# Kernel tuning notes

Hardware: AMD Instinct MI355X
Metric: run time of the kernel (lower is better)

## Reference

```python
import jax, jax.numpy as jnp
import numpy as np

N_USERS = 100000
N_ITEMS = 100000
D_FEAT = 256
BATCH = 8192
CLASSES = 5
E = 500000
D_CONV = 128
D_RAW = 256
D_EMB = 256
NUM_BASIS = 2
BN_EPS = 1e-3  # tf.contrib.layers.batch_norm default epsilon


def _bn_params(key, dim):
    # packed [gamma, beta, moving_mean, moving_var]
    return jnp.stack([jnp.ones(dim), jnp.zeros(dim), jnp.zeros(dim), jnp.ones(dim)]).astype(jnp.float32)


def setup_inputs() -> dict:
    key = jax.random.key(0)
    ks = jax.random.split(key, 24)
    s = lambda fan_in, fan_out: np.sqrt(2.0 / (fan_in + fan_out)).astype(np.float32)
    inp = {
        'user_feat': jax.random.normal(ks[0], (N_USERS, D_FEAT), jnp.float32),
        'item_feat': jax.random.normal(ks[1], (N_ITEMS, D_FEAT), jnp.float32),
        'user_idx': jax.random.randint(ks[2], (BATCH,), 0, N_USERS, jnp.int32),
        'item_idx': jax.random.randint(ks[3], (BATCH,), 0, N_ITEMS, jnp.int32),
        'user_edge_src': jax.random.randint(ks[4], (CLASSES, E), 0, N_ITEMS, jnp.int32),
        'user_edge_dst': jax.random.randint(ks[5], (CLASSES, E), 0, BATCH, jnp.int32),
        'user_edge_w': jax.random.uniform(ks[6], (CLASSES, E), jnp.float32),
        'item_edge_src': jax.random.randint(ks[7], (CLASSES, E), 0, N_USERS, jnp.int32),
        'item_edge_dst': jax.random.randint(ks[8], (CLASSES, E), 0, BATCH, jnp.int32),
        'item_edge_w': jax.random.uniform(ks[9], (CLASSES, E), jnp.float32),
        'W_fu': jax.random.normal(ks[10], (D_FEAT, D_RAW), jnp.float32) * s(D_FEAT, D_RAW),
        'b_fu': jnp.zeros((D_RAW,), jnp.float32),
        'W_fi': jax.random.normal(ks[11], (D_FEAT, D_RAW), jnp.float32) * s(D_FEAT, D_RAW),
        'b_fi': jnp.zeros((D_RAW,), jnp.float32),
        'W_uc': jax.random.normal(ks[12], (CLASSES, D_FEAT, D_CONV), jnp.float32) * s(D_FEAT, D_CONV),
        'W_ic': jax.random.normal(ks[13], (CLASSES, D_FEAT, D_CONV), jnp.float32) * s(D_FEAT, D_CONV),
        'bn_fu': _bn_params(ks[14], D_RAW),
        'bn_hu': _bn_params(ks[15], CLASSES * D_CONV),
        'bn_fi': _bn_params(ks[16], D_RAW),
        'bn_hi': _bn_params(ks[17], CLASSES * D_CONV),
        'W2_fu': jax.random.normal(ks[18], (D_RAW, D_EMB), jnp.float32) * s(D_RAW, D_EMB),
        'W2_hu': jax.random.normal(ks[19], (CLASSES * D_CONV, D_EMB), jnp.float32) * s(CLASSES * D_CONV, D_EMB),
        'W2_fi': jax.random.normal(ks[20], (D_RAW, D_EMB), jnp.float32) * s(D_RAW, D_EMB),
        'W2_hi': jax.random.normal(ks[21], (CLASSES * D_CONV, D_EMB), jnp.float32) * s(CLASSES * D_CONV, D_EMB),
        'Wdec': jax.random.normal(ks[22], (NUM_BASIS, D_EMB, D_EMB), jnp.float32) * s(D_EMB, D_EMB),
        'Wcomb': jax.random.normal(ks[23], (CLASSES, NUM_BASIS), jnp.float32) * s(CLASSES, NUM_BASIS),
    }
    return inp


def _bn(x, p):
    gamma, beta, mean, var = p[0], p[1], p[2], p[3]
    return gamma * (x - mean) * jax.lax.rsqrt(var + BN_EPS) + beta


def _agg(feat, src, dst, w, n_rows):
    # weighted sparse [B, N] x dense [N, D] aggregation via gather + segment_sum
    msgs = feat[src] * w[:, None]  # [E, D]
    return jax.ops.segment_sum(msgs, dst, num_segments=n_rows)


def reference(user_feat, item_feat, user_idx, item_idx,
              user_edge_src, user_edge_dst, user_edge_w,
              item_edge_src, item_edge_dst, item_edge_w,
              W_fu, b_fu, W_fi, b_fi, W_uc, W_ic,
              bn_fu, bn_hu, bn_fi, bn_hi,
              W2_fu, W2_hu, W2_fi, W2_hi, Wdec, Wcomb):
    B = user_idx.shape[0]
    classes = W_uc.shape[0]

    # batch row selection (sparse.matmul with one-hot selector == gather)
    f_user = user_feat[user_idx] @ W_fu + b_fu  # [B, D_RAW]
    f_item = item_feat[item_idx] @ W_fi + b_fi

    # per-class graph convolution: aggregate opposite-side features, project, stack
    h_user = jnp.concatenate(
        [_agg(item_feat, user_edge_src[c], user_edge_dst[c], user_edge_w[c], B) @ W_uc[c]
         for c in range(classes)], axis=1)  # [B, classes*D_CONV]
    h_item = jnp.concatenate(
        [_agg(user_feat, item_edge_src[c], item_edge_dst[c], item_edge_w[c], B) @ W_ic[c]
         for c in range(classes)], axis=1)

    # batchnorm (inference stats) + relu  (dropout rate 0 -> identity)
    f_user = jax.nn.relu(_bn(f_user, bn_fu))
    f_item = jax.nn.relu(_bn(f_item, bn_fi))
    h_user = jax.nn.relu(_bn(h_user, bn_hu))
    h_item = jax.nn.relu(_bn(h_item, bn_hi))

    user_emb = jax.nn.relu(f_user @ W2_fu + h_user @ W2_hu)  # [B, D_EMB]
    item_emb = jax.nn.relu(f_item @ W2_fi + h_item @ W2_hi)

    # bilinear decoder: per-class kernel = sum_k Wcomb[r,k] * Wdec[k]
    kernels = jnp.einsum('rk,kij->rij', Wcomb, Wdec)  # [classes, D_EMB, D_EMB]
    logits = jnp.einsum('bi,rij,bj->br', user_emb, kernels, item_emb)  # [B, classes]
    return logits


if __name__ == '__main__':
    out = reference(**setup_inputs())
    print(out.shape, out.dtype)
```

## Files before the change

### kernel.cpp

```cpp
#include <hip/hip_runtime.h>
#include <cstdint>
#include <cstddef>

#define NBATCH   8192
#define DFEAT    256
#define DCONV    128
#define NCLASS   5
#define NEDGE    500000
#define NUSERS   100000
#define BN_EPS   1e-3f
#define NBUCKET  128
#define BROWS    64
#define CAP      4608
#define NPHB     16
#define NPHU     13

typedef unsigned short u16;
typedef short bf16x8_t __attribute__((ext_vector_type(8)));
typedef float f32x4_t  __attribute__((ext_vector_type(4)));

__device__ __forceinline__ u16 f2bf(float x) {
    unsigned u = __float_as_uint(x);
    u += 0x7FFF + ((u >> 16) & 1);
    return (u16)(u >> 16);
}
__device__ __forceinline__ float bf2f(u16 h) {
    return __uint_as_float(((unsigned)h) << 16);
}

template<int AF32>
__device__ __forceinline__ void mfma_tiles_t(
    const void* __restrict__ Av, int lda, const int* __restrict__ gather,
    const u16* __restrict__ BT, int K,
    int tileM, int tileN, u16* As, u16* Bs, f32x4_t acc[4])
{
    const int t    = threadIdx.x;
    const int rowi = t >> 2;
    const int kc   = t & 3;
    const int w    = t >> 6;
    const int lane = t & 63;

    int ar = gather ? gather[tileM + rowi] : (tileM + rowi);
    const u16*   Ap16 = (const u16*)Av   + (size_t)ar * lda + kc * 8;
    const float* Apf  = (const float*)Av + (size_t)ar * lda + kc * 8;
    const u16* Bp = BT + (size_t)(tileN + rowi) * K + kc * 8;
    u16* Aw = As + (size_t)(((rowi >> 4) * 64) + (rowi & 15) + 16 * kc) * 8;
    u16* Bw = Bs + (size_t)(((rowi >> 4) * 64) + (rowi & 15) + 16 * kc) * 8;
    const u16* Ar = As + (size_t)(w * 64 + lane) * 8;

    for (int k0 = 0; k0 < K; k0 += 32) {
        __syncthreads();
        if (AF32) {
            float4 a0 = *(const float4*)(Apf + k0);
            float4 a1 = *(const float4*)(Apf + k0 + 4);
            ushort4 p0, p1;
            p0.x = f2bf(a0.x); p0.y = f2bf(a0.y); p0.z = f2bf(a0.z); p0.w = f2bf(a0.w);
            p1.x = f2bf(a1.x); p1.y = f2bf(a1.y); p1.z = f2bf(a1.z); p1.w = f2bf(a1.w);
            *(ushort4*)Aw = p0;
            *(ushort4*)(Aw + 4) = p1;
        } else {
            *(uint4*)Aw = *(const uint4*)(Ap16 + k0);
        }
        *(uint4*)Bw = *(const uint4*)(Bp + k0);
        __syncthreads();
        bf16x8_t av = *(const bf16x8_t*)Ar;
        #pragma unroll
        for (int nb = 0; nb < 4; ++nb) {
            bf16x8_t bv = *(const bf16x8_t*)(Bs + (size_t)(nb * 64 + lane) * 8);
            acc[nb] = __builtin_amdgcn_mfma_f32_16x16x32_bf16(av, bv, acc[nb], 0, 0, 0);
        }
    }
}

__device__ __forceinline__ void epilogue(
    f32x4_t acc[4], int tileM, int tileN,
    const float* __restrict__ bias, const float* __restrict__ bn, int bn_ld,
    int relu, u16* __restrict__ out_bf, float* __restrict__ out_f32, int ldc)
{
    const int t = threadIdx.x, w = t >> 6, lane = t & 63;
    const int row0 = tileM + w * 16 + (lane >> 4) * 4;
    #pragma unroll
    for (int nb = 0; nb < 4; ++nb) {
        int col = tileN + nb * 16 + (lane & 15);
        float g = 1.f, be = 0.f, mu = 0.f, va = 1.f, bs = 0.f;
        if (bn)   { g = bn[col]; be = bn[bn_ld + col]; mu = bn[2 * bn_ld + col]; va = bn[3 * bn_ld + col]; }
        if (bias) bs = bias[col];
        #pragma unroll
        for (int r = 0; r < 4; ++r) {
            float x = acc[nb][r] + bs;
            if (bn)   x = g * (x - mu) * rsqrtf(va + BN_EPS) + be;
            if (relu) x = fmaxf(x, 0.f);
            size_t o = (size_t)(row0 + r) * ldc + col;
            if (out_bf) out_bf[o] = f2bf(x);
            else        out_f32[o] = x;
        }
    }
}

__global__ __launch_bounds__(256) void k_fh(
    const float* __restrict__ uf, const float* __restrict__ itf,
    const int* __restrict__ uidx, const int* __restrict__ iidx,
    const u16* __restrict__ WTu, const u16* __restrict__ WTi,
    const float* __restrict__ bu, const float* __restrict__ bi,
    const float* __restrict__ bnu, const float* __restrict__ bni,
    u16* __restrict__ outu, u16* __restrict__ outi,
    const u16* __restrict__ agg, const u16* __restrict__ WucT, const u16* __restrict__ WicT,
    const float* __restrict__ bn_hu, const float* __restrict__ bn_hi,
    u16* __restrict__ h_user, u16* __restrict__ h_item)
{
    __shared__ __align__(16) u16 As[2048], Bs[2048];
    f32x4_t z4 = {0.f, 0.f, 0.f, 0.f};
    f32x4_t acc[4] = {z4, z4, z4, z4};
    int id = blockIdx.x;
    if (id < 1024) {
        int z  = id >> 9;
        int ny = (id >> 7) & 3;
        int mx = id & 127;
        const float* feat = z ? itf : uf;
        const int* idx  = z ? iidx : uidx;
        const u16* WT   = z ? WTi : WTu;
        const float* bias = z ? bi : bu;
        const float* bn   = z ? bni : bnu;
        u16* out = z ? outi : outu;
        int tileM = mx * 64, tileN = ny * 64;
        mfma_tiles_t<1>(feat, 256, idx, WT, 256, tileM, tileN, As, Bs, acc);
        epilogue(acc, tileM, tileN, bias, bn, 256, 1, out, nullptr, 256);
    } else {
        int r  = id - 1024;
        int cs = r >> 8;
        int ny = (r >> 7) & 1;
        int mx = r & 127;
        int c = cs % NCLASS, side = cs / NCLASS;
        const u16* A  = agg + (size_t)cs * NBATCH * DFEAT;
        const u16* BT = (side ? WicT : WucT) + (size_t)c * DCONV * DFEAT;
        const float* bn = (side ? bn_hi : bn_hu) + c * DCONV;
        u16* out = (side ? h_item : h_user) + c * DCONV;
        int tileM = mx * 64, tileN = ny * 64;
        mfma_tiles_t<0>(A, 256, nullptr, BT, 256, tileM, tileN, As, Bs, acc);
        epilogue(acc, tileM, tileN, nullptr, bn, NCLASS * DCONV, 1, out, nullptr, NCLASS * DCONV);
    }
}

__global__ __launch_bounds__(256) void k_emb(
    const u16* __restrict__ fu, const u16* __restrict__ fi,
    const u16* __restrict__ hu, const u16* __restrict__ hi,
    const u16* __restrict__ W2fTu, const u16* __restrict__ W2hTu,
    const u16* __restrict__ W2fTi, const u16* __restrict__ W2hTi,
    u16* __restrict__ embu, u16* __restrict__ embi)
{
    __shared__ __align__(16) u16 As[2048], Bs[2048];
    f32x4_t z4 = {0.f, 0.f, 0.f, 0.f};
    f32x4_t acc[4] = {z4, z4, z4, z4};
    int z = blockIdx.z;
    const u16* fbf  = z ? fi : fu;
    const u16* hbf  = z ? hi : hu;
    const u16* W2fT = z ? W2fTi : W2fTu;
    const u16* W2hT = z ? W2hTi : W2hTu;
    u16* emb = z ? embi : embu;
    int tileM = blockIdx.x * 64, tileN = blockIdx.y * 64;
    mfma_tiles_t<0>(fbf, 256, nullptr, W2fT, 256, tileM, tileN, As, Bs, acc);
    mfma_tiles_t<0>(hbf, NCLASS * DCONV, nullptr, W2hT, NCLASS * DCONV, tileM, tileN, As, Bs, acc);
    epilogue(acc, tileM, tileN, nullptr, nullptr, 0, 1, emb, nullptr, 256);
}

__global__ __launch_bounds__(256) void k_dec(
    const u16* __restrict__ emb, const u16* __restrict__ WdecT,
    float* __restrict__ t0, float* __restrict__ t1)
{
    __shared__ __align__(16) u16 As[2048], Bs[2048];
    f32x4_t z4 = {0.f, 0.f, 0.f, 0.f};
    f32x4_t acc[4] = {z4, z4, z4, z4};
    int zi = blockIdx.z;
    const u16* BT = WdecT + (size_t)zi * 256 * 256;
    float* out = zi ? t1 : t0;
    int tileM = blockIdx.x * 64, tileN = blockIdx.y * 64;
    mfma_tiles_t<0>(emb, 256, nullptr, BT, 256, tileM, tileN, As, Bs, acc);
    epilogue(acc, tileM, tileN, nullptr, nullptr, 0, 0, nullptr, out, 256);
}

#define OFF_WFU   0
#define OFF_WFI   65536
#define OFF_WUC   131072
#define OFF_WIC   294912
#define OFF_W2FU  458752
#define OFF_W2HU  524288
#define OFF_W2FI  688128
#define OFF_W2HI  753664
#define OFF_WDEC  917504

__global__ __launch_bounds__(256) void prep_all(
    const int* __restrict__ u_src, const int* __restrict__ u_dst, const float* __restrict__ u_w,
    const int* __restrict__ i_src, const int* __restrict__ i_dst, const float* __restrict__ i_w,
    int* __restrict__ bcur, uint2* __restrict__ part,
    const float* __restrict__ uf, const float* __restrict__ itf,
    u16* __restrict__ ubf, u16* __restrict__ ibf,
    const float* __restrict__ Wfu, const float* __restrict__ Wfi,
    const float* __restrict__ Wuc, const float* __restrict__ Wic,
    const float* __restrict__ W2fu, const float* __restrict__ W2hu,
    const float* __restrict__ W2fi, const float* __restrict__ W2hi,
    const float* __restrict__ Wdec, u16* __restrict__ wT)
{
    __shared__ union {
        struct { int hist[NBUCKET]; int cur[NBUCKET]; } p;
        float tile[32][33];
    } sm;
    int id = blockIdx.x;
    if (id < 1280) {
        int cs = id / 128;
        int bx = id - cs * 128;
        const int* srcp; const int* dstp; const float* wp;
        if (cs < NCLASS) {
            srcp = u_src + (size_t)cs * NEDGE;
            dstp = u_dst + (size_t)cs * NEDGE;
            wp   = u_w   + (size_t)cs * NEDGE;
        } else {
            int c = cs - NCLASS;
            srcp = i_src + (size_t)c * NEDGE;
            dstp = i_dst + (size_t)c * NEDGE;
            wp   = i_w   + (size_t)c * NEDGE;
        }
        int lo_e = (int)(((long long)bx * NEDGE) >> 7);
        int hi_e = (int)(((long long)(bx + 1) * NEDGE) >> 7);

        for (int i = threadIdx.x; i < NBUCKET; i += 256) sm.p.hist[i] = 0;
        __syncthreads();
        for (int e = lo_e + threadIdx.x; e < hi_e; e += 256)
            atomicAdd(&sm.p.hist[dstp[e] >> 6], 1);
        __syncthreads();
        for (int i = threadIdx.x; i < NBUCKET; i += 256)
            sm.p.cur[i] = atomicAdd(&bcur[cs * NBUCKET + i], sm.p.hist[i]);
        __syncthreads();
        uint2* out = part + (size_t)cs * NBUCKET * CAP;
        for (int e = lo_e + threadIdx.x; e < hi_e; e += 256) {
            int dst = dstp[e];
            int bkt = dst >> 6;
            int pos = atomicAdd(&sm.p.cur[bkt], 1);
            if (pos < bkt * CAP + CAP)
                out[pos] = make_uint2((unsigned)srcp[e] | ((unsigned)(dst & 63) << 24),
                                      __float_as_uint(wp[e]));
        }
    } else if (id < 1280 + 4096) {
        int bx = id - 1280;
        const size_t n4 = (size_t)NUSERS * DFEAT / 4;
        for (size_t i = (size_t)bx * 256 + threadIdx.x; i < 2 * n4;
             i += (size_t)4096 * 256) {
            bool u = i < n4;
            size_t j = u ? i : i - n4;
            float4 v = u ? ((const float4*)uf)[j] : ((const float4*)itf)[j];
            ushort4 o;
            o.x = f2bf(v.x); o.y = f2bf(v.y); o.z = f2bf(v.z); o.w = f2bf(v.w);
            ((ushort4*)(u ? ubf : ibf))[j] = o;
        }
    } else {
        int r0 = id - (1280 + 4096);
        int cse = r0 / 160;
        int tid = r0 - cse * 160;
        const float* in; u16* out; int K, N, B;
        switch (cse) {
            case 0: in = Wfu;  out = wT + OFF_WFU;  K = 256; N = 256; B = 1; break;
            case 1: in = Wfi;  out = wT + OFF_WFI;  K = 256; N = 256; B = 1; break;
            case 2: in = Wuc;  out = wT + OFF_WUC;  K = 256; N = 128; B = 5; break;
            case 3: in = Wic;  out = wT + OFF_WIC;  K = 256; N = 128; B = 5; break;
            case 4: in = W2fu; out = wT + OFF_W2FU; K = 256; N = 256; B = 1; break;
            case 5: in = W2hu; out = wT + OFF_W2HU; K = 640; N = 256; B = 1; break;
            case 6: in = W2fi; out = wT + OFF_W2FI; K = 256; N = 256; B = 1; break;
            case 7: in = W2hi; out = wT + OFF_W2HI; K = 640; N = 256; B = 1; break;
            default: in = Wdec; out = wT + OFF_WDEC; K = 256; N = 256; B = 2; break;
        }
        int tk = K >> 5, tn = N >> 5;
        if (tid >= B * tk * tn) return;
        int b  = tid / (tk * tn);
        int r  = tid - b * tk * tn;
        int kt = r % tk, nt = r / tk;
        int k0 = kt * 32, n0 = nt * 32;
        int ty = threadIdx.x >> 5, tx = threadIdx.x & 31;
        const float* ip = in + (size_t)b * K * N;
        u16* op = out + (size_t)b * N * K;
        #pragma unroll
        for (int i = 0; i < 4; ++i) {
            int row = ty + 8 * i;
            sm.tile[row][tx] = ip[(size_t)(k0 + row) * N + (n0 + tx)];
        }
        __syncthreads();
        #pragma unroll
        for (int i = 0; i < 4; ++i) {
            int row = ty + 8 * i;
            op[(size_t)(n0 + row) * K + (k0 + tx)] = f2bf(sm.tile[tx][row]);
        }
    }
}

__global__ __launch_bounds__(256) void init_bcur(int* __restrict__ bcur)
{
    int i = blockIdx.x * 256 + threadIdx.x;
    if (i < 10 * NBUCKET) bcur[i] = (i & (NBUCKET - 1)) * CAP;
}

__device__ __forceinline__ int edge_key(unsigned x) {
    return (int)((x >> 24) * NPHB) + (int)((x & 0xFFFFFFu) >> 13);
}

__global__ __launch_bounds__(512) void spmm_sorted(
    const u16* __restrict__ item_bf, const u16* __restrict__ user_bf,
    const uint2* __restrict__ part, const int* __restrict__ bcur,
    u16* __restrict__ agg)
{
    __shared__ int bin_cnt[BROWS * NPHB];
    __shared__ int bin_off[BROWS * NPHB + 1];
    __shared__ int bin_cur[BROWS * NPHB];
    __shared__ int wsum[8];
    __shared__ __align__(8) uint2 sorted[CAP];
    int id   = blockIdx.x;
    int side = id & 1;
    int k    = id >> 1;
    int c    = k >> 7;
    int b    = k & 127;
    int cs   = side * NCLASS + c;
    const u16* feat = side ? user_bf : item_bf;
    int n = bcur[cs * NBUCKET + b] - b * CAP;
    if (n > CAP) n = CAP;
    const uint2* ew = part + ((size_t)cs * NBUCKET + b) * CAP;
    int tid = threadIdx.x, wave = tid >> 6, lane = tid & 63;

    bin_cnt[tid] = 0;
    bin_cnt[tid + 512] = 0;
    __syncthreads();
    for (int e = tid; e < n; e += 512)
        atomicAdd(&bin_cnt[edge_key(ew[e].x)], 1);
    __syncthreads();
    {
        int i2 = tid * 2;
        int c0 = bin_cnt[i2], c1 = bin_cnt[i2 + 1];
        int s = c0 + c1;
        int v = s;
        #pragma unroll
        for (int o = 1; o < 64; o <<= 1) {
            int u = __shfl_up(v, o);
            if (lane >= o) v += u;
        }
        if (lane == 63) wsum[wave] = v;
        __syncthreads();
        if (tid < 8) {
            int s8 = wsum[tid];
            #pragma unroll
            for (int o = 1; o < 8; o <<= 1) {
                int u = __shfl_up(s8, o);
                if (lane >= o) s8 += u;
            }
            wsum[tid] = s8;
        }
        __syncthreads();
        int base = (wave ? wsum[wave - 1] : 0) + (v - s);
        bin_off[i2] = base;
        bin_off[i2 + 1] = base + c0;
        bin_cur[i2] = base;
        bin_cur[i2 + 1] = base + c0;
        if (tid == 511) bin_off[1024] = base + s;
    }
    __syncthreads();
    for (int e = tid; e < n; e += 512) {
        uint2 p = ew[e];
        int pos = atomicAdd(&bin_cur[edge_key(p.x)], 1);
        sorted[pos] = p;
    }
    __syncthreads();

    int rowbase = cs * NBATCH + b * BROWS;
    float ax[8], ay[8], az[8], aw[8];
    #pragma unroll
    for (int r0 = 0; r0 < 8; ++r0) { ax[r0] = 0.f; ay[r0] = 0.f; az[r0] = 0.f; aw[r0] = 0.f; }

    #pragma unroll
    for (int r0 = 0; r0 < 8; ++r0) {
        int base = (wave * 8 + r0) * NPHB;
        int j0 = bin_off[base], j1 = bin_off[base + NPHU];
        int j = j0;
        for (; j + 7 < j1; j += 8) {
            uint2 p[8];
            #pragma unroll
            for (int q = 0; q < 8; ++q) p[q] = sorted[j + q];
            ushort4 v[8];
            #pragma unroll
            for (int q = 0; q < 8; ++q)
                v[q] = *(const ushort4*)&feat[(size_t)(p[q].x & 0xFFFFFF) * DFEAT + lane * 4];
            #pragma unroll
            for (int q = 0; q < 8; ++q) {
                float w = __uint_as_float(p[q].y);
                ax[r0] += w * bf2f(v[q].x);
                ay[r0] += w * bf2f(v[q].y);
                az[r0] += w * bf2f(v[q].z);
                aw[r0] += w * bf2f(v[q].w);
            }
        }
        for (; j + 3 < j1; j += 4) {
            uint2 p0 = sorted[j], p1 = sorted[j + 1], p2 = sorted[j + 2], p3 = sorted[j + 3];
            ushort4 v0 = *(const ushort4*)&feat[(size_t)(p0.x & 0xFFFFFF) * DFEAT + lane * 4];
            ushort4 v1 = *(const ushort4*)&feat[(size_t)(p1.x & 0xFFFFFF) * DFEAT + lane * 4];
            ushort4 v2 = *(const ushort4*)&feat[(size_t)(p2.x & 0xFFFFFF) * DFEAT + lane * 4];
            ushort4 v3 = *(const ushort4*)&feat[(size_t)(p3.x & 0xFFFFFF) * DFEAT + lane * 4];
            float w0 = __uint_as_float(p0.y), w1 = __uint_as_float(p1.y);
            float w2 = __uint_as_float(p2.y), w3 = __uint_as_float(p3.y);
            ax[r0] += w0 * bf2f(v0.x) + w1 * bf2f(v1.x) + w2 * bf2f(v2.x) + w3 * bf2f(v3.x);
            ay[r0] += w0 * bf2f(v0.y) + w1 * bf2f(v1.y) + w2 * bf2f(v2.y) + w3 * bf2f(v3.y);
            az[r0] += w0 * bf2f(v0.z) + w1 * bf2f(v1.z) + w2 * bf2f(v2.z) + w3 * bf2f(v3.z);
            aw[r0] += w0 * bf2f(v0.w) + w1 * bf2f(v1.w) + w2 * bf2f(v2.w) + w3 * bf2f(v3.w);
        }
        for (; j < j1; ++j) {
            uint2 p0 = sorted[j];
            ushort4 v0 = *(const ushort4*)&feat[(size_t)(p0.x & 0xFFFFFF) * DFEAT + lane * 4];
            float w0 = __uint_as_float(p0.y);
            ax[r0] += w0 * bf2f(v0.x);
            ay[r0] += w0 * bf2f(v0.y);
            az[r0] += w0 * bf2f(v0.z);
            aw[r0] += w0 * bf2f(v0.w);
        }
    }

    #pragma unroll
    for (int r0 = 0; r0 < 8; ++r0) {
        ushort4 o4;
        o4.x = f2bf(ax[r0]); o4.y = f2bf(ay[r0]); o4.z = f2bf(az[r0]); o4.w = f2bf(aw[r0]);
        *(ushort4*)&agg[(size_t)(rowbase + wave * 8 + r0) * 256 + lane * 4] = o4;
    }
}

__global__ __launch_bounds__(256) void decoder_kernel(
    const float* __restrict__ t0, const float* __restrict__ t1,
    const u16* __restrict__ item_emb, const float* __restrict__ Wcomb,
    float* __restrict__ out)
{
    int wave = threadIdx.x >> 6;
    int lane = threadIdx.x & 63;
    int b = blockIdx.x * 4 + wave;
    const u16*   ie = item_emb + (size_t)b * 256;
    const float* p0 = t0 + (size_t)b * 256;
    const float* p1 = t1 + (size_t)b * 256;
    float s0 = 0.f, s1 = 0.f;
    #pragma unroll
    for (int j = lane; j < 256; j += 64) {
        float v = bf2f(ie[j]);
        s0 += p0[j] * v;
        s1 += p1[j] * v;
    }
    #pragma unroll
    for (int o = 32; o > 0; o >>= 1) {
        s0 += __shfl_down(s0, o);
        s1 += __shfl_down(s1, o);
    }
    if (lane == 0) {
        #pragma unroll
        for (int r = 0; r < NCLASS; ++r)
            out[b * NCLASS + r] = Wcomb[r * 2 + 0] * s0 + Wcomb[r * 2 + 1] * s1;
    }
}

extern "C" void kernel_launch(void* const* d_in, const int* in_sizes, int n_in,
                              void* d_out, int out_size, void* d_ws, size_t ws_size,
                              hipStream_t stream)
{
    const float* user_feat = (const float*)d_in[0];
    const float* item_feat = (const float*)d_in[1];
    const int*   user_idx  = (const int*)  d_in[2];
    const int*   item_idx  = (const int*)  d_in[3];
    const int*   u_src     = (const int*)  d_in[4];
    const int*   u_dst     = (const int*)  d_in[5];
    const float* u_w       = (const float*)d_in[6];
    const int*   i_src     = (const int*)  d_in[7];
    const int*   i_dst     = (const int*)  d_in[8];
    const float* i_w       = (const float*)d_in[9];
    const float* W_fu      = (const float*)d_in[10];
    const float* b_fu      = (const float*)d_in[11];
    const float* W_fi      = (const float*)d_in[12];
    const float* b_fi      = (const float*)d_in[13];
    const float* W_uc      = (const float*)d_in[14];
    const float* W_ic      = (const float*)d_in[15];
    const float* bn_fu     = (const float*)d_in[16];
    const float* bn_hu     = (const float*)d_in[17];
    const float* bn_fi     = (const float*)d_in[18];
    const float* bn_hi     = (const float*)d_in[19];
    const float* W2_fu     = (const float*)d_in[20];
    const float* W2_hu     = (const float*)d_in[21];
    const float* W2_fi     = (const float*)d_in[22];
    const float* W2_hi     = (const float*)d_in[23];
    const float* Wdec      = (const float*)d_in[24];
    const float* Wcomb     = (const float*)d_in[25];
    float* out = (float*)d_out;

    char* ws = (char*)d_ws;
    int*   bcur       = (int*)  (ws + 0);
    uint2* part_ew    = (uint2*)(ws + 65536);
    u16*   user_bf    = (u16*)  (ws + 47251456);
    u16*   item_bf    = (u16*)  (ws + 98451456);
    u16*   agg_bf     = (u16*)  (ws + 149651456);
    u16*   wT         = (u16*)  (ws + 191594496);
    u16*   f_user_bf  = (u16*)  (ws + 65536);
    u16*   f_item_bf  = (u16*)  (ws + 4259840);
    u16*   h_user_bf  = (u16*)  (ws + 8454144);
    u16*   h_item_bf  = (u16*)  (ws + 18939904);
    float* t0         = (float*)(ws + 149651456);
    float* t1         = (float*)(ws + 158040064);
    u16*   user_emb   = (u16*)  (ws + 166428672);
    u16*   item_emb   = (u16*)  (ws + 170622976);

    init_bcur<<<5, 256, 0, stream>>>(bcur);
    prep_all<<<6816, 256, 0, stream>>>(
        u_src, u_dst, u_w, i_src, i_dst, i_w, bcur, part_ew,
        user_feat, item_feat, user_bf, item_bf,
        W_fu, W_fi, W_uc, W_ic, W2_fu, W2_hu, W2_fi, W2_hi, Wdec, wT);

    spmm_sorted<<<dim3(2 * NCLASS * NBUCKET), 512, 0, stream>>>(
        item_bf, user_bf, part_ew, bcur, agg_bf);

    k_fh<<<3584, 256, 0, stream>>>(
        user_feat, item_feat, user_idx, item_idx, wT + OFF_WFU, wT + OFF_WFI,
        b_fu, b_fi, bn_fu, bn_fi, f_user_bf, f_item_bf,
        agg_bf, wT + OFF_WUC, wT + OFF_WIC, bn_hu, bn_hi, h_user_bf, h_item_bf);

    k_emb<<<dim3(128, 4, 2), 256, 0, stream>>>(
        f_user_bf, f_item_bf, h_user_bf, h_item_bf,
        wT + OFF_W2FU, wT + OFF_W2HU, wT + OFF_W2FI, wT + OFF_W2HI,
        user_emb, item_emb);

    k_dec<<<dim3(128, 4, 2), 256, 0, stream>>>(user_emb, wT + OFF_WDEC, t0, t1);
    decoder_kernel<<<NBATCH / 4, 256, 0, stream>>>(t0, t1, item_emb, Wcomb, out);
}
```

Before: 762.5 us.

## Iterate aggregation by source-phase bins across rows to improve feature locality

Reorders the gather-accumulate loop so that all waves sweep source-index phase bins in lockstep. Each wave handles its 8 rows one phase at a time instead of processing each row's full edge list before moving on. Concurrent gathers then hit a narrower slice of the feature table, which should improve L2/MALL hit rates. Tail handling becomes clamped, zero-weighted padding to groups of 4, which wastes some loads on short bins and gives up the 8-wide unroll.

```diff
diff --git a/kernel.cpp b/kernel.cpp
--- a/kernel.cpp
+++ b/kernel.cpp
@@ -370,49 +370,33 @@
     #pragma unroll
     for (int r0 = 0; r0 < 8; ++r0) { ax[r0] = 0.f; ay[r0] = 0.f; az[r0] = 0.f; aw[r0] = 0.f; }
 
-    #pragma unroll
-    for (int r0 = 0; r0 < 8; ++r0) {
-        int base = (wave * 8 + r0) * NPHB;
-        int j0 = bin_off[base], j1 = bin_off[base + NPHU];
-        int j = j0;
-        for (; j + 7 < j1; j += 8) {
-            uint2 p[8];
-            #pragma unroll
-            for (int q = 0; q < 8; ++q) p[q] = sorted[j + q];
-            ushort4 v[8];
-            #pragma unroll
-            for (int q = 0; q < 8; ++q)
-                v[q] = *(const ushort4*)&feat[(size_t)(p[q].x & 0xFFFFFF) * DFEAT + lane * 4];
-            #pragma unroll
-            for (int q = 0; q < 8; ++q) {
-                float w = __uint_as_float(p[q].y);
-                ax[r0] += w * bf2f(v[q].x);
-                ay[r0] += w * bf2f(v[q].y);
-                az[r0] += w * bf2f(v[q].z);
-                aw[r0] += w * bf2f(v[q].w);
+    for (int ph = 0; ph < NPHU; ++ph) {
+        #pragma unroll
+        for (int r0 = 0; r0 < 8; ++r0) {
+            int bi = (wave * 8 + r0) * NPHB + ph;
+            int j0 = bin_off[bi], j1 = bin_off[bi + 1];
+            for (int j = j0; j < j1; j += 4) {
+                uint2 p[4];
+                float w[4];
+                #pragma unroll
+                for (int q = 0; q < 4; ++q) {
+                    int jj = j + q;
+                    int jc = jj < j1 ? jj : j1 - 1;
+                    p[q] = sorted[jc];
+                    w[q] = jj < j1 ? __uint_as_float(p[q].y) : 0.f;
+                }
+                ushort4 v[4];
+                #pragma unroll
+                for (int q = 0; q < 4; ++q)
+                    v[q] = *(const ushort4*)&feat[(size_t)(p[q].x & 0xFFFFFF) * DFEAT + lane * 4];
+                #pragma unroll
+                for (int q = 0; q < 4; ++q) {
+                    ax[r0] += w[q] * bf2f(v[q].x);
+                    ay[r0] += w[q] * bf2f(v[q].y);
+                    az[r0] += w[q] * bf2f(v[q].z);
+                    aw[r0] += w[q] * bf2f(v[q].w);
+                }
             }
-        }
-        for (; j + 3 < j1; j += 4) {
-            uint2 p0 = sorted[j], p1 = sorted[j + 1], p2 = sorted[j + 2], p3 = sorted[j + 3];
-            ushort4 v0 = *(const ushort4*)&feat[(size_t)(p0.x & 0xFFFFFF) * DFEAT + lane * 4];
-            ushort4 v1 = *(const ushort4*)&feat[(size_t)(p1.x & 0xFFFFFF) * DFEAT + lane * 4];
-            ushort4 v2 = *(const ushort4*)&feat[(size_t)(p2.x & 0xFFFFFF) * DFEAT + lane * 4];
-            ushort4 v3 = *(const ushort4*)&feat[(size_t)(p3.x & 0xFFFFFF) * DFEAT + lane * 4];
-            float w0 = __uint_as_float(p0.y), w1 = __uint_as_float(p1.y);
-            float w2 = __uint_as_float(p2.y), w3 = __uint_as_float(p3.y);
-            ax[r0] += w0 * bf2f(v0.x) + w1 * bf2f(v1.x) + w2 * bf2f(v2.x) + w3 * bf2f(v3.x);
-            ay[r0] += w0 * bf2f(v0.y) + w1 * bf2f(v1.y) + w2 * bf2f(v2.y) + w3 * bf2f(v3.y);
-            az[r0] += w0 * bf2f(v0.z) + w1 * bf2f(v1.z) + w2 * bf2f(v2.z) + w3 * bf2f(v3.z);
-            aw[r0] += w0 * bf2f(v0.w) + w1 * bf2f(v1.w) + w2 * bf2f(v2.w) + w3 * bf2f(v3.w);
-        }
-        for (; j < j1; ++j) {
-            uint2 p0 = sorted[j];
-            ushort4 v0 = *(const ushort4*)&feat[(size_t)(p0.x & 0xFFFFFF) * DFEAT + lane * 4];
-            float w0 = __uint_as_float(p0.y);
-            ax[r0] += w0 * bf2f(v0.x);
-            ay[r0] += w0 * bf2f(v0.y);
-            az[r0] += w0 * bf2f(v0.z);
-            aw[r0] += w0 * bf2f(v0.w);
         }
     }
 
```

After: 696.2 us. 8.7% less time.
